# Kernel tuning notes

Hardware: AMD Instinct MI355X
Metric: run time of the kernel (lower is better)

The kernel has to match this reference:

```python
import jax, jax.numpy as jnp
import numpy as np

N_EMBD = 768
N_HEAD = 12
HEAD_DIM = N_EMBD // N_HEAD


def setup_inputs() -> dict:
    key = jax.random.key(0)
    ks = jax.random.split(key, 5)
    B, T, C = 1, 4096, N_EMBD
    s = 1.0 / np.sqrt(C)
    return {
        "x": jax.random.normal(ks[0], (B, T, C), dtype=jnp.float32),
        "wq": jax.random.normal(ks[1], (C, C), dtype=jnp.float32) * s,
        "wk": jax.random.normal(ks[2], (C, C), dtype=jnp.float32) * s,
        "wv": jax.random.normal(ks[3], (C, C), dtype=jnp.float32) * s,
        "wo": jax.random.normal(ks[4], (C, C), dtype=jnp.float32) * s,
    }


def reference(x, wq, wk, wv, wo):
    B, T, C = x.shape
    H, D = N_HEAD, HEAD_DIM
    # projections: torch Linear(y = x @ W^T); weights stored as (out, in)
    q = (x @ wq.T).reshape(B, T, H, D).transpose(0, 2, 1, 3)  # B H T D
    k = (x @ wk.T).reshape(B, T, H, D).transpose(0, 2, 1, 3)
    v = (x @ wv.T).reshape(B, T, H, D).transpose(0, 2, 1, 3)
    scale = 1.0 / jnp.sqrt(jnp.asarray(D, dtype=x.dtype))
    attn = jnp.einsum("bhtd,bhsd->bhts", q, k) * scale  # B H T T
    causal = jnp.tril(jnp.ones((T, T), dtype=bool))
    attn = jnp.where(causal, attn, -jnp.inf)
    attn = jax.nn.softmax(attn, axis=-1)
    out = jnp.einsum("bhts,bhsd->bhtd", attn, v)  # B H T D
    out = out.transpose(0, 2, 1, 3).reshape(B, T, C)
    return out @ wo.T
```

## Files before the change

### kernel.cpp

```cpp
#include <hip/hip_runtime.h>


#define T_SEQ 4096
#define C_EMB 768
#define NH    12
#define HD    64

typedef __attribute__((ext_vector_type(8))) short bf16x8;
typedef __attribute__((ext_vector_type(4))) float floatx4;

#define QSCALE 0.18033688011112042f

__device__ __forceinline__ unsigned short f2bf(float f) {
  union { float f; unsigned u; } v; v.f = f;
  unsigned r = v.u + 0x7fffu + ((v.u >> 16) & 1u);
  return (unsigned short)(r >> 16);
}
__device__ __forceinline__ unsigned short f2bf_rhu(float f) {
  union { float f; unsigned u; } v; v.f = f;
  return (unsigned short)((v.u + 0x8000u) >> 16);
}
__device__ __forceinline__ float bf2f(unsigned short h) {
  union { unsigned u; float f; } v; v.u = ((unsigned)h) << 16;
  return v.f;
}

__device__ __forceinline__ void gload_lds16(const void* gptr, void* ldsptr) {
  __builtin_amdgcn_global_load_lds(
      (const __attribute__((address_space(1))) unsigned int*)gptr,
      (__attribute__((address_space(3))) unsigned int*)ldsptr,
      16, 0, 0);
}

__global__ void cast_all_kernel(const float* __restrict__ x,
                                const float* __restrict__ wq,
                                const float* __restrict__ wk,
                                const float* __restrict__ wv,
                                const float* __restrict__ wo,
                                unsigned short* __restrict__ dst) {
  const int GX = (T_SEQ * C_EMB) / 4;
  const int GW = (C_EMB * C_EMB) / 4;
  int i = blockIdx.x * blockDim.x + threadIdx.x;
  const float* src; int local;
  if (i < GX) { src = x; local = i; }
  else {
    int t = i - GX; int w = t / GW; local = t - w * GW;
    src = (w == 0) ? wq : (w == 1) ? wk : (w == 2) ? wv : wo;
  }
  float4 f = reinterpret_cast<const float4*>(src)[local];
  ushort4 u;
  u.x = f2bf(f.x); u.y = f2bf(f.y); u.z = f2bf(f.z); u.w = f2bf(f.w);
  reinterpret_cast<ushort4*>(dst)[i] = u;
}

__global__ __launch_bounds__(256) void gemm_qkv(
    const unsigned short* __restrict__ A,
    const unsigned short* __restrict__ B,
    unsigned short* __restrict__ Qb,
    unsigned short* __restrict__ Kb,
    unsigned short* __restrict__ Vt) {
  constexpr int K = 768, BM = 64, BN = 128, BK = 64;
  __shared__ __align__(16) unsigned short As[BM * BK];
  __shared__ __align__(16) unsigned short Bs[BN * BK];
  const int tid = threadIdx.x;
  const int wave = tid >> 6, lane = tid & 63;
  const int lm = lane & 15, lq = lane >> 4;
  const int swz = lm & 7;
  const int m0 = blockIdx.x * BM, n0 = blockIdx.y * BN;
  const int wm = (wave & 1) * 32, wn = (wave >> 1) * 64;
  floatx4 acc[2][4] = {};

  for (int k0 = 0; k0 < K; k0 += BK) {
#pragma unroll
    for (int i = 0; i < 2; i++) {
      int idx = i * 256 + tid;
      int row = idx >> 3;
      int ch = (idx & 7) ^ (row & 7);
      gload_lds16(A + (size_t)(m0 + row) * K + k0 + ch * 8, (char*)As + idx * 16);
    }
#pragma unroll
    for (int i = 0; i < 4; i++) {
      int idx = i * 256 + tid;
      int row = idx >> 3;
      int ch = (idx & 7) ^ (row & 7);
      gload_lds16(B + (size_t)(n0 + row) * K + k0 + ch * 8, (char*)Bs + idx * 16);
    }
    __syncthreads();
#pragma unroll
    for (int kk = 0; kk < 2; kk++) {
      bf16x8 af[2], bfr[4];
#pragma unroll
      for (int i = 0; i < 2; i++) {
        int row = wm + i * 16 + lm;
        af[i] = *(const bf16x8*)(As + row * BK + (((kk * 4 + lq) ^ swz) * 8));
      }
#pragma unroll
      for (int j = 0; j < 4; j++) {
        int row = wn + j * 16 + lm;
        bfr[j] = *(const bf16x8*)(Bs + row * BK + (((kk * 4 + lq) ^ swz) * 8));
      }
#pragma unroll
      for (int i = 0; i < 2; i++)
#pragma unroll
        for (int j = 0; j < 4; j++)
          acc[i][j] = __builtin_amdgcn_mfma_f32_16x16x32_bf16(af[i], bfr[j], acc[i][j], 0, 0, 0);
    }
    __syncthreads();
  }

  const int which = n0 / C_EMB;
  if (which < 2) {
    unsigned short* tgt = (which == 0) ? Qb : Kb;
    const float sc = (which == 0) ? QSCALE : 1.0f;
#pragma unroll
    for (int i = 0; i < 2; i++)
#pragma unroll
      for (int j = 0; j < 4; j++) {
        int n = n0 - which * C_EMB + wn + j * 16 + lm;
        int h = n >> 6, d = n & 63;
#pragma unroll
        for (int r = 0; r < 4; r++) {
          int m = m0 + wm + i * 16 + lq * 4 + r;
          tgt[(((size_t)h * T_SEQ + m) << 6) + d] = f2bf(acc[i][j][r] * sc);
        }
      }
  } else {
#pragma unroll
    for (int i = 0; i < 2; i++)
#pragma unroll
      for (int j = 0; j < 4; j++) {
        int n = n0 - 2 * C_EMB + wn + j * 16 + lm;
        int h = n >> 6, d = n & 63;
        int m = m0 + wm + i * 16 + lq * 4;
        ushort4 pk;
        pk.x = f2bf(acc[i][j][0]); pk.y = f2bf(acc[i][j][1]);
        pk.z = f2bf(acc[i][j][2]); pk.w = f2bf(acc[i][j][3]);
        *(ushort4*)(Vt + ((size_t)(h * HD + d)) * T_SEQ + m) = pk;
      }
  }
}

struct AttnState {
  float rsum[2][4];
  floatx4 o_acc[2][4];
};

template <typename EpilogueFn>
__device__ __forceinline__ void attn_body(
    const unsigned short* __restrict__ Q,
    const unsigned short* __restrict__ K,
    const unsigned short* __restrict__ Vt,
    int h, int q0, int sb, int se,
    unsigned short* Ks, unsigned short* Vs, unsigned short* Ps,
    EpilogueFn epi) {
  constexpr int BS = 64, PS = 72;
  const int tid = threadIdx.x;
  const int wave = tid >> 6, lane = tid & 63;
  const int lm = lane & 15, lq = lane >> 4;
  const unsigned short* Qh = Q + (size_t)h * T_SEQ * HD;
  const unsigned short* Kh = K + (size_t)h * T_SEQ * HD;
  const unsigned short* Vh = Vt + (size_t)h * HD * T_SEQ;
  const int qrow_base = q0 + wave * 32;
  unsigned short* Pw = Ps + wave * 32 * PS;
  const int swz = lm & 7;

  bf16x8 qf[2][2];
#pragma unroll
  for (int m = 0; m < 2; m++)
#pragma unroll
    for (int kk = 0; kk < 2; kk++)
      qf[m][kk] = *(const bf16x8*)(Qh + (size_t)(qrow_base + m * 16 + lm) * HD + kk * 32 + lq * 8);

  AttnState st;
#pragma unroll
  for (int m = 0; m < 2; m++)
#pragma unroll
    for (int r = 0; r < 4; r++) { st.rsum[m][r] = 0.f; st.o_acc[m][r] = floatx4{0.f,0.f,0.f,0.f}; }

  auto stage = [&](int s0) {
#pragma unroll
    for (int i = 0; i < 2; i++) {
      int idx = (wave * 2 + i) * 64 + lane;
      int row = idx >> 3;
      int ch = (idx & 7) ^ (row & 7);
      gload_lds16(Kh + (size_t)(s0 + row) * HD + ch * 8, (char*)Ks + idx * 16);
      gload_lds16(Vh + (size_t)row * T_SEQ + s0 + ch * 8, (char*)Vs + idx * 16);
    }
  };

  stage(sb * BS);
  for (int it = sb; it < se; ++it) {
    const int s0 = it * BS;
    __syncthreads();

    floatx4 sa[2][4] = {};
#pragma unroll
    for (int kk = 0; kk < 2; kk++)
#pragma unroll
      for (int j = 0; j < 4; j++) {
        int row = j * 16 + lm;
        bf16x8 kf = *(const bf16x8*)(Ks + (row * 8 + ((kk * 4 + lq) ^ swz)) * 8);
#pragma unroll
        for (int m = 0; m < 2; m++)
          sa[m][j] = __builtin_amdgcn_mfma_f32_16x16x32_bf16(qf[m][kk], kf, sa[m][j], 0, 0, 0);
      }

    if (s0 >= q0) {
#pragma unroll
      for (int m = 0; m < 2; m++)
#pragma unroll
        for (int j = 0; j < 4; j++) {
          int scol = s0 + j * 16 + lm;
#pragma unroll
          for (int r = 0; r < 4; r++) {
            int qrow = qrow_base + m * 16 + lq * 4 + r;
            if (scol > qrow) sa[m][j][r] = -1e30f;
          }
        }
    }

#pragma unroll
    for (int m = 0; m < 2; m++)
#pragma unroll
      for (int j = 0; j < 4; j++)
#pragma unroll
        for (int r = 0; r < 4; r++) {
          float p = __builtin_amdgcn_exp2f(sa[m][j][r]);
          st.rsum[m][r] += p;
          Pw[(m * 16 + lq * 4 + r) * PS + j * 16 + lm] = f2bf_rhu(p);
        }

#pragma unroll
    for (int kk = 0; kk < 2; kk++) {
      bf16x8 pf[2];
#pragma unroll
      for (int m = 0; m < 2; m++)
        pf[m] = *(const bf16x8*)(Pw + (m * 16 + lm) * PS + kk * 32 + lq * 8);
#pragma unroll
      for (int jd = 0; jd < 4; jd++) {
        int row = jd * 16 + lm;
        bf16x8 vf = *(const bf16x8*)(Vs + (row * 8 + ((kk * 4 + lq) ^ swz)) * 8);
#pragma unroll
        for (int m = 0; m < 2; m++)
          st.o_acc[m][jd] = __builtin_amdgcn_mfma_f32_16x16x32_bf16(pf[m], vf, st.o_acc[m][jd], 0, 0, 0);
      }
    }

    if (it + 1 < se) {
      __syncthreads();
      stage(s0 + BS);
    }
  }

#pragma unroll
  for (int m = 0; m < 2; m++)
#pragma unroll
    for (int r = 0; r < 4; r++) {
      float s = st.rsum[m][r];
      s += __shfl_xor(s, 1);
      s += __shfl_xor(s, 2);
      s += __shfl_xor(s, 4);
      s += __shfl_xor(s, 8);
      st.rsum[m][r] = s;
    }
  epi(st, qrow_base, lm, lq);
}

__global__ __launch_bounds__(256, 4) void attn_kernel2(
    const unsigned short* __restrict__ Q,
    const unsigned short* __restrict__ K,
    const unsigned short* __restrict__ Vt,
    unsigned short* __restrict__ Op0,
    unsigned short* __restrict__ Op1,
    float* __restrict__ lpart) {
  constexpr int BS = 64, PS = 72;
  __shared__ __align__(16) unsigned short Ks[BS * HD];
  __shared__ __align__(16) unsigned short Vs[HD * BS];
  __shared__ __align__(16) unsigned short Ps[4 * 32 * PS];
  const int bid = blockIdx.x;
  const int h = bid % NH;
  const int z = bid / NH;
  const int qt = (T_SEQ / 128 - 1) - (z >> 1);
  const int c = z & 1;
  const int q0 = qt * 128;
  const int sb = c ? (qt + 1) : 0;
  const int se = c ? (2 * qt + 2) : (qt + 1);

  unsigned short* Oc = c ? Op1 : Op0;
  float* lc = lpart + (size_t)c * NH * T_SEQ;
  attn_body(Q, K, Vt, h, q0, sb, se, Ks, Vs, Ps,
    [&](const AttnState& st, int qrow_base, int lm, int lq) {
#pragma unroll
      for (int m = 0; m < 2; m++)
#pragma unroll
        for (int r = 0; r < 4; r++) {
          int t = qrow_base + m * 16 + lq * 4 + r;
          if (lm == 0) lc[h * T_SEQ + t] = st.rsum[m][r];
#pragma unroll
          for (int jd = 0; jd < 4; jd++)
            Oc[((size_t)h * T_SEQ + t) * HD + jd * 16 + lm] = f2bf(st.o_acc[m][jd][r]);
        }
    });
}

__global__ void combine_kernel2(const unsigned short* __restrict__ Op0,
                                const unsigned short* __restrict__ Op1,
                                const float* __restrict__ lpart,
                                unsigned short* __restrict__ Ob) {
  int idx = blockIdx.x * blockDim.x + threadIdx.x;
  int d4 = idx & 15;
  int t = (idx >> 4) & (T_SEQ - 1);
  int h = idx >> 16;
  float l = lpart[h * T_SEQ + t] + lpart[NH * T_SEQ + h * T_SEQ + t];
  float inv = 1.0f / l;
  ushort4 a = reinterpret_cast<const ushort4*>(Op0)[idx];
  ushort4 b = reinterpret_cast<const ushort4*>(Op1)[idx];
  ushort4 u;
  u.x = f2bf((bf2f(a.x) + bf2f(b.x)) * inv);
  u.y = f2bf((bf2f(a.y) + bf2f(b.y)) * inv);
  u.z = f2bf((bf2f(a.z) + bf2f(b.z)) * inv);
  u.w = f2bf((bf2f(a.w) + bf2f(b.w)) * inv);
  *(ushort4*)(Ob + (size_t)t * C_EMB + h * HD + d4 * 4) = u;
}

__global__ __launch_bounds__(256, 4) void attn_kernel4(
    const unsigned short* __restrict__ Q,
    const unsigned short* __restrict__ K,
    const unsigned short* __restrict__ Vt,
    float* __restrict__ Opart,
    float* __restrict__ lpart) {
  constexpr int BS = 64, PS = 72;
  __shared__ __align__(16) unsigned short Ks[BS * HD];
  __shared__ __align__(16) unsigned short Vs[HD * BS];
  __shared__ __align__(16) unsigned short Ps[4 * 32 * PS];
  const int bid = blockIdx.x;
  const int h = bid % NH;
  const int z = bid / NH;
  const int qt = (T_SEQ / 128 - 1) - (z >> 2);
  const int c = z & 3;
  const int q0 = qt * 128;
  const int n = 2 * qt + 2;
  const int sb = (n * c) >> 2, se = (n * (c + 1)) >> 2;
  if (sb == se) return;

  const size_t CN = (size_t)NH * T_SEQ * HD;
  float* Oc = Opart + (size_t)c * CN;
  float* lc = lpart + (size_t)c * NH * T_SEQ;
  attn_body(Q, K, Vt, h, q0, sb, se, Ks, Vs, Ps,
    [&](const AttnState& st, int qrow_base, int lm, int lq) {
#pragma unroll
      for (int m = 0; m < 2; m++)
#pragma unroll
        for (int r = 0; r < 4; r++) {
          int t = qrow_base + m * 16 + lq * 4 + r;
          if (lm == 0) lc[h * T_SEQ + t] = st.rsum[m][r];
#pragma unroll
          for (int jd = 0; jd < 4; jd++)
            Oc[((size_t)h * T_SEQ + t) * HD + jd * 16 + lm] = st.o_acc[m][jd][r];
        }
    });
}

__global__ void combine_kernel4(const float* __restrict__ Opart,
                                const float* __restrict__ lpart,
                                unsigned short* __restrict__ Ob) {
  int idx = blockIdx.x * blockDim.x + threadIdx.x;
  int d4 = idx & 15;
  int t = (idx >> 4) & (T_SEQ - 1);
  int h = idx >> 16;
  const int qt = t >> 7;
  const int n = 2 * qt + 2;
  const size_t CN4 = (size_t)NH * T_SEQ * HD / 4;
  float4 o = make_float4(0.f, 0.f, 0.f, 0.f);
  float l = 0.f;
#pragma unroll
  for (int c = 0; c < 4; c++) {
    if (((n * c) >> 2) != ((n * (c + 1)) >> 2)) {
      float4 p = reinterpret_cast<const float4*>(Opart)[c * CN4 + idx];
      o.x += p.x; o.y += p.y; o.z += p.z; o.w += p.w;
      l += lpart[c * NH * T_SEQ + h * T_SEQ + t];
    }
  }
  float inv = 1.0f / l;
  ushort4 u;
  u.x = f2bf(o.x * inv); u.y = f2bf(o.y * inv);
  u.z = f2bf(o.z * inv); u.w = f2bf(o.w * inv);
  *(ushort4*)(Ob + (size_t)t * C_EMB + h * HD + d4 * 4) = u;
}

__global__ __launch_bounds__(256) void gemm_out(
    const unsigned short* __restrict__ A,
    const unsigned short* __restrict__ B,
    float* __restrict__ Out) {
  constexpr int K = 768, BM = 64, BN = 128, BK = 64;
  __shared__ __align__(16) unsigned short As[BM * BK];
  __shared__ __align__(16) unsigned short Bs[BN * BK];
  const int tid = threadIdx.x;
  const int wave = tid >> 6, lane = tid & 63;
  const int lm = lane & 15, lq = lane >> 4;
  const int swz = lm & 7;
  const int m0 = blockIdx.x * BM, n0 = blockIdx.y * BN;
  const int wm = (wave & 1) * 32, wn = (wave >> 1) * 64;
  floatx4 acc[2][4] = {};

  for (int k0 = 0; k0 < K; k0 += BK) {
#pragma unroll
    for (int i = 0; i < 2; i++) {
      int idx = i * 256 + tid;
      int row = idx >> 3;
      int ch = (idx & 7) ^ (row & 7);
      gload_lds16(A + (size_t)(m0 + row) * K + k0 + ch * 8, (char*)As + idx * 16);
    }
#pragma unroll
    for (int i = 0; i < 4; i++) {
      int idx = i * 256 + tid;
      int row = idx >> 3;
      int ch = (idx & 7) ^ (row & 7);
      gload_lds16(B + (size_t)(n0 + row) * K + k0 + ch * 8, (char*)Bs + idx * 16);
    }
    __syncthreads();
#pragma unroll
    for (int kk = 0; kk < 2; kk++) {
      bf16x8 af[2], bfr[4];
#pragma unroll
      for (int i = 0; i < 2; i++) {
        int row = wm + i * 16 + lm;
        af[i] = *(const bf16x8*)(As + row * BK + (((kk * 4 + lq) ^ swz) * 8));
      }
#pragma unroll
      for (int j = 0; j < 4; j++) {
        int row = wn + j * 16 + lm;
        bfr[j] = *(const bf16x8*)(Bs + row * BK + (((kk * 4 + lq) ^ swz) * 8));
      }
#pragma unroll
      for (int i = 0; i < 2; i++)
#pragma unroll
        for (int j = 0; j < 4; j++)
          acc[i][j] = __builtin_amdgcn_mfma_f32_16x16x32_bf16(af[i], bfr[j], acc[i][j], 0, 0, 0);
    }
    __syncthreads();
  }
#pragma unroll
  for (int i = 0; i < 2; i++)
#pragma unroll
    for (int j = 0; j < 4; j++)
#pragma unroll
      for (int r = 0; r < 4; r++) {
        int m = m0 + wm + i * 16 + lq * 4 + r;
        int n = n0 + wn + j * 16 + lm;
        Out[(size_t)m * C_EMB + n] = acc[i][j][r];
      }
}

extern "C" void kernel_launch(void* const* d_in, const int* in_sizes, int n_in,
                              void* d_out, int out_size, void* d_ws, size_t ws_size,
                              hipStream_t stream) {
  const float* x  = (const float*)d_in[0];
  const float* wq = (const float*)d_in[1];
  const float* wk = (const float*)d_in[2];
  const float* wv = (const float*)d_in[3];
  const float* wo = (const float*)d_in[4];
  float* out = (float*)d_out;

  const size_t XN = (size_t)T_SEQ * C_EMB;
  const size_t WN = (size_t)C_EMB * C_EMB;
  unsigned short* base = (unsigned short*)d_ws;

  unsigned short* Xb   = base;
  unsigned short* Wqkv = base + XN;
  unsigned short* Wob  = base + XN + 3 * WN;
  unsigned short* Qb   = base + XN + 4 * WN;
  unsigned short* Kb   = Qb + XN;
  unsigned short* Vt   = Kb + XN;
  unsigned short* tail = Vt + XN;
  unsigned short* Ob   = Qb;

  const size_t needA = 29884416ull + 4ull * XN * 4ull + 4ull * NH * T_SEQ * 4ull;

  const int ngroups = (int)((XN + 4 * WN) / 4);
  cast_all_kernel<<<dim3(ngroups / 256), 256, 0, stream>>>(x, wq, wk, wv, wo, Xb);

  gemm_qkv<<<dim3(T_SEQ / 64, 2304 / 128), 256, 0, stream>>>(Xb, Wqkv, Qb, Kb, Vt);

  if (ws_size >= needA) {
    float* Opart4 = (float*)tail;
    float* lpart4 = Opart4 + 4 * XN;
    attn_kernel4<<<dim3((T_SEQ / 128) * 4 * NH), 256, 0, stream>>>(Qb, Kb, Vt, Opart4, lpart4);
    combine_kernel4<<<dim3((int)(XN / 4) / 256), 256, 0, stream>>>(Opart4, lpart4, Ob);
  } else {
    unsigned short* Op0 = base;
    unsigned short* Op1 = tail;
    float* lpart = (float*)(base + XN);
    attn_kernel2<<<dim3((T_SEQ / 128) * 2 * NH), 256, 0, stream>>>(Qb, Kb, Vt, Op0, Op1, lpart);
    combine_kernel2<<<dim3((int)(XN / 4) / 256), 256, 0, stream>>>(Op0, Op1, lpart, Ob);
  }

  gemm_out<<<dim3(T_SEQ / 64, C_EMB / 128), 256, 0, stream>>>(Ob, Wob, out);
}
```

Before: 166.7 us.

## Double attention key block to 128 and rebalance split-KV partitions

Raises the key/value tile staged in LDS per iteration from 64 to 128 rows. Each staged tile is processed as two 64-column halves, and the V tile gets a 16-way XOR swizzle for its wider rows. This halves the number of barrier and stage rounds per query tile. The split-KV partition counts and the combine kernels are rewritten for the new block count, and launch bounds drop to 3 blocks per CU. The cost is more LDS per block and lower occupancy, and the split partitions become coarser and less balanced.

```diff
diff --git a/kernel.cpp b/kernel.cpp
--- a/kernel.cpp
+++ b/kernel.cpp
@@ -153,7 +153,7 @@
     int h, int q0, int sb, int se,
     unsigned short* Ks, unsigned short* Vs, unsigned short* Ps,
     EpilogueFn epi) {
-  constexpr int BS = 64, PS = 72;
+  constexpr int BS = 128, PS = 72;
   const int tid = threadIdx.x;
   const int wave = tid >> 6, lane = tid & 63;
   const int lm = lane & 15, lq = lane >> 4;
@@ -179,11 +179,17 @@
 
   auto stage = [&](int s0) {
 #pragma unroll
-    for (int i = 0; i < 2; i++) {
-      int idx = (wave * 2 + i) * 64 + lane;
+    for (int i = 0; i < 4; i++) {
+      int idx = (wave * 4 + i) * 64 + lane;
       int row = idx >> 3;
       int ch = (idx & 7) ^ (row & 7);
       gload_lds16(Kh + (size_t)(s0 + row) * HD + ch * 8, (char*)Ks + idx * 16);
+    }
+#pragma unroll
+    for (int i = 0; i < 4; i++) {
+      int idx = (wave * 4 + i) * 64 + lane;
+      int row = idx >> 4;
+      int ch = (idx & 15) ^ (row & 15);
       gload_lds16(Vh + (size_t)row * T_SEQ + s0 + ch * 8, (char*)Vs + idx * 16);
     }
   };
@@ -193,56 +199,61 @@
     const int s0 = it * BS;
     __syncthreads();
 
-    floatx4 sa[2][4] = {};
-#pragma unroll
-    for (int kk = 0; kk < 2; kk++)
-#pragma unroll
-      for (int j = 0; j < 4; j++) {
-        int row = j * 16 + lm;
-        bf16x8 kf = *(const bf16x8*)(Ks + (row * 8 + ((kk * 4 + lq) ^ swz)) * 8);
+#pragma unroll
+    for (int hb = 0; hb < 2; hb++) {
+      const int sh0 = s0 + hb * 64;
+
+      floatx4 sa[2][4] = {};
+#pragma unroll
+      for (int kk = 0; kk < 2; kk++)
+#pragma unroll
+        for (int j = 0; j < 4; j++) {
+          int row = hb * 64 + j * 16 + lm;
+          bf16x8 kf = *(const bf16x8*)(Ks + (row * 8 + ((kk * 4 + lq) ^ swz)) * 8);
+#pragma unroll
+          for (int m = 0; m < 2; m++)
+            sa[m][j] = __builtin_amdgcn_mfma_f32_16x16x32_bf16(qf[m][kk], kf, sa[m][j], 0, 0, 0);
+        }
+
+      if (sh0 >= q0 - 64) {
 #pragma unroll
         for (int m = 0; m < 2; m++)
-          sa[m][j] = __builtin_amdgcn_mfma_f32_16x16x32_bf16(qf[m][kk], kf, sa[m][j], 0, 0, 0);
-      }
-
-    if (s0 >= q0) {
+#pragma unroll
+          for (int j = 0; j < 4; j++) {
+            int scol = sh0 + j * 16 + lm;
+#pragma unroll
+            for (int r = 0; r < 4; r++) {
+              int qrow = qrow_base + m * 16 + lq * 4 + r;
+              if (scol > qrow) sa[m][j][r] = -1e30f;
+            }
+          }
+      }
+
 #pragma unroll
       for (int m = 0; m < 2; m++)
 #pragma unroll
-        for (int j = 0; j < 4; j++) {
-          int scol = s0 + j * 16 + lm;
+        for (int j = 0; j < 4; j++)
 #pragma unroll
           for (int r = 0; r < 4; r++) {
-            int qrow = qrow_base + m * 16 + lq * 4 + r;
-            if (scol > qrow) sa[m][j][r] = -1e30f;
+            float p = __builtin_amdgcn_exp2f(sa[m][j][r]);
+            st.rsum[m][r] += p;
+            Pw[(m * 16 + lq * 4 + r) * PS + j * 16 + lm] = f2bf_rhu(p);
           }
+
+#pragma unroll
+      for (int kk = 0; kk < 2; kk++) {
+        bf16x8 pf[2];
+#pragma unroll
+        for (int m = 0; m < 2; m++)
+          pf[m] = *(const bf16x8*)(Pw + (m * 16 + lm) * PS + kk * 32 + lq * 8);
+#pragma unroll
+        for (int jd = 0; jd < 4; jd++) {
+          int row = jd * 16 + lm;
+          bf16x8 vf = *(const bf16x8*)(Vs + (row * 16 + ((hb * 8 + kk * 4 + lq) ^ lm)) * 8);
+#pragma unroll
+          for (int m = 0; m < 2; m++)
+            st.o_acc[m][jd] = __builtin_amdgcn_mfma_f32_16x16x32_bf16(pf[m], vf, st.o_acc[m][jd], 0, 0, 0);
         }
-    }
-
-#pragma unroll
-    for (int m = 0; m < 2; m++)
-#pragma unroll
-      for (int j = 0; j < 4; j++)
-#pragma unroll
-        for (int r = 0; r < 4; r++) {
-          float p = __builtin_amdgcn_exp2f(sa[m][j][r]);
-          st.rsum[m][r] += p;
-          Pw[(m * 16 + lq * 4 + r) * PS + j * 16 + lm] = f2bf_rhu(p);
-        }
-
-#pragma unroll
-    for (int kk = 0; kk < 2; kk++) {
-      bf16x8 pf[2];
-#pragma unroll
-      for (int m = 0; m < 2; m++)
-        pf[m] = *(const bf16x8*)(Pw + (m * 16 + lm) * PS + kk * 32 + lq * 8);
-#pragma unroll
-      for (int jd = 0; jd < 4; jd++) {
-        int row = jd * 16 + lm;
-        bf16x8 vf = *(const bf16x8*)(Vs + (row * 8 + ((kk * 4 + lq) ^ swz)) * 8);
-#pragma unroll
-        for (int m = 0; m < 2; m++)
-          st.o_acc[m][jd] = __builtin_amdgcn_mfma_f32_16x16x32_bf16(pf[m], vf, st.o_acc[m][jd], 0, 0, 0);
       }
     }
 
@@ -266,16 +277,16 @@
   epi(st, qrow_base, lm, lq);
 }
 
-__global__ __launch_bounds__(256, 4) void attn_kernel2(
+__global__ __launch_bounds__(256, 3) void attn_kernel2(
     const unsigned short* __restrict__ Q,
     const unsigned short* __restrict__ K,
     const unsigned short* __restrict__ Vt,
     unsigned short* __restrict__ Op0,
     unsigned short* __restrict__ Op1,
     float* __restrict__ lpart) {
-  constexpr int BS = 64, PS = 72;
-  __shared__ __align__(16) unsigned short Ks[BS * HD];
-  __shared__ __align__(16) unsigned short Vs[HD * BS];
+  constexpr int PS = 72;
+  __shared__ __align__(16) unsigned short Ks[128 * HD];
+  __shared__ __align__(16) unsigned short Vs[HD * 128];
   __shared__ __align__(16) unsigned short Ps[4 * 32 * PS];
   const int bid = blockIdx.x;
   const int h = bid % NH;
@@ -283,8 +294,9 @@
   const int qt = (T_SEQ / 128 - 1) - (z >> 1);
   const int c = z & 1;
   const int q0 = qt * 128;
-  const int sb = c ? (qt + 1) : 0;
-  const int se = c ? (2 * qt + 2) : (qt + 1);
+  const int n = qt + 1;
+  const int sb = (n * c) >> 1, se = (n * (c + 1)) >> 1;
+  if (sb == se) return;
 
   unsigned short* Oc = c ? Op1 : Op0;
   float* lc = lpart + (size_t)c * NH * T_SEQ;
@@ -311,27 +323,34 @@
   int d4 = idx & 15;
   int t = (idx >> 4) & (T_SEQ - 1);
   int h = idx >> 16;
-  float l = lpart[h * T_SEQ + t] + lpart[NH * T_SEQ + h * T_SEQ + t];
+  const int qt = t >> 7;
+  const int n = qt + 1;
+  float o[4] = {0.f, 0.f, 0.f, 0.f};
+  float l = 0.f;
+#pragma unroll
+  for (int c = 0; c < 2; c++) {
+    if (((n * c) >> 1) != ((n * (c + 1)) >> 1)) {
+      ushort4 a = reinterpret_cast<const ushort4*>(c ? Op1 : Op0)[idx];
+      o[0] += bf2f(a.x); o[1] += bf2f(a.y); o[2] += bf2f(a.z); o[3] += bf2f(a.w);
+      l += lpart[c * NH * T_SEQ + h * T_SEQ + t];
+    }
+  }
   float inv = 1.0f / l;
-  ushort4 a = reinterpret_cast<const ushort4*>(Op0)[idx];
-  ushort4 b = reinterpret_cast<const ushort4*>(Op1)[idx];
   ushort4 u;
-  u.x = f2bf((bf2f(a.x) + bf2f(b.x)) * inv);
-  u.y = f2bf((bf2f(a.y) + bf2f(b.y)) * inv);
-  u.z = f2bf((bf2f(a.z) + bf2f(b.z)) * inv);
-  u.w = f2bf((bf2f(a.w) + bf2f(b.w)) * inv);
+  u.x = f2bf(o[0] * inv); u.y = f2bf(o[1] * inv);
+  u.z = f2bf(o[2] * inv); u.w = f2bf(o[3] * inv);
   *(ushort4*)(Ob + (size_t)t * C_EMB + h * HD + d4 * 4) = u;
 }
 
-__global__ __launch_bounds__(256, 4) void attn_kernel4(
+__global__ __launch_bounds__(256, 3) void attn_kernel4(
     const unsigned short* __restrict__ Q,
     const unsigned short* __restrict__ K,
     const unsigned short* __restrict__ Vt,
     float* __restrict__ Opart,
     float* __restrict__ lpart) {
-  constexpr int BS = 64, PS = 72;
-  __shared__ __align__(16) unsigned short Ks[BS * HD];
-  __shared__ __align__(16) unsigned short Vs[HD * BS];
+  constexpr int PS = 72;
+  __shared__ __align__(16) unsigned short Ks[128 * HD];
+  __shared__ __align__(16) unsigned short Vs[HD * 128];
   __shared__ __align__(16) unsigned short Ps[4 * 32 * PS];
   const int bid = blockIdx.x;
   const int h = bid % NH;
@@ -339,7 +358,7 @@
   const int qt = (T_SEQ / 128 - 1) - (z >> 2);
   const int c = z & 3;
   const int q0 = qt * 128;
-  const int n = 2 * qt + 2;
+  const int n = qt + 1;
   const int sb = (n * c) >> 2, se = (n * (c + 1)) >> 2;
   if (sb == se) return;
 
@@ -369,7 +388,7 @@
   int t = (idx >> 4) & (T_SEQ - 1);
   int h = idx >> 16;
   const int qt = t >> 7;
-  const int n = 2 * qt + 2;
+  const int n = qt + 1;
   const size_t CN4 = (size_t)NH * T_SEQ * HD / 4;
   float4 o = make_float4(0.f, 0.f, 0.f, 0.f);
   float l = 0.f;
```

After: 168.2 us. About the same (+0.9%).
